# Kernel optimization log

Measured on AMD Instinct MI355X. Metric: run time of the kernel, lower is better.

Reference implementation:

```python
import jax, jax.numpy as jnp
import numpy as np

EPS = 1e-5
MAX_NORM = 1.0 - EPS
K = 16
ALPHA = 0.1
TAU = 0.1  # softmax temperature in forward


def project(x):
    # enforce ||x|| < 1 on the Poincare ball
    n = jnp.clip(jnp.linalg.norm(x, axis=-1, keepdims=True), EPS, None)
    return x / jnp.maximum(n / MAX_NORM, 1.0)


def mobius_add(u, v):
    c = 1.0
    dot_uv = jnp.sum(u * v, axis=-1, keepdims=True)
    nu = jnp.clip(jnp.sum(u * u, axis=-1, keepdims=True), 0.0, MAX_NORM ** 2)
    nv = jnp.clip(jnp.sum(v * v, axis=-1, keepdims=True), 0.0, MAX_NORM ** 2)
    num = (1 + 2 * c * dot_uv + c * nv) * u + (1 - c * nu) * v
    den = 1 + 2 * c * dot_uv + c * c * nu * nv
    return project(num / jnp.clip(den, EPS, None))


def exp_map(x, v):
    # sqrt_c = 1
    vn = jnp.clip(jnp.linalg.norm(v, axis=-1, keepdims=True), EPS, None)
    second = jnp.tanh(vn / 2.0) * v / vn
    return mobius_add(x, second)


def poincare_cdist(q, mem):
    # q: [B, M], mem: [N, M] -> [B, N] geodesic distances (c=1)
    qn = jnp.clip(jnp.sum(q * q, axis=-1), 0.0, MAX_NORM ** 2)          # [B]
    mn = jnp.clip(jnp.sum(mem * mem, axis=-1), 0.0, MAX_NORM ** 2)      # [N]
    # ||q - m||^2 expanded via gram matrix (same math as diff-based form)
    dist_sq = jnp.clip(jnp.sum(q * q, axis=-1)[:, None] + jnp.sum(mem * mem, axis=-1)[None, :]
                       - 2.0 * q @ mem.T, 0.0, None)                     # [B, N]
    den = (1.0 - qn)[:, None] * (1.0 - mn)[None, :]
    x = 2.0 * dist_sq / jnp.clip(den, EPS, None)
    return jnp.arccosh(1.0 + x)


def layernorm(x, g, b):
    mu = jnp.mean(x, axis=-1, keepdims=True)
    var = jnp.mean((x - mu) ** 2, axis=-1, keepdims=True)
    return (x - mu) / jnp.sqrt(var + 1e-5) * g + b


def setup_inputs() -> dict:
    key = jax.random.key(0)
    ks = jax.random.split(key, 10)
    B, S, H, M, N = 32, 2048, 1024, 128, 500000
    hidden_states = jax.random.normal(ks[0], (B, S, H), dtype=jnp.float32)
    W1 = jax.random.normal(ks[1], (H, M), dtype=jnp.float32) * 0.02
    b1 = jnp.zeros((M,), dtype=jnp.float32)
    ln_g = jnp.ones((M,), dtype=jnp.float32)
    ln_b = jnp.zeros((M,), dtype=jnp.float32)
    W2 = jax.random.normal(ks[2], (M, M), dtype=jnp.float32) * 0.02
    b2 = jnp.zeros((M,), dtype=jnp.float32)
    q_origin = jnp.zeros((1, M), dtype=jnp.float32)
    memory = project(jax.random.normal(ks[3], (N, M), dtype=jnp.float32) * 0.3)
    Wp = jax.random.normal(ks[4], (M, H), dtype=jnp.float32) * 0.02
    bp = jnp.zeros((H,), dtype=jnp.float32)
    return {"hidden_states": hidden_states, "W1": W1, "b1": b1, "ln_g": ln_g,
            "ln_b": ln_b, "W2": W2, "b2": b2, "q_origin": q_origin,
            "memory": memory, "Wp": Wp, "bp": bp}


def reference(hidden_states, W1, b1, ln_g, ln_b, W2, b2, q_origin, memory, Wp, bp):
    B, S, H = hidden_states.shape
    # query network on mean-pooled hidden states
    pooled = jnp.mean(hidden_states, axis=1)                  # [B, H]
    h = pooled @ W1 + b1                                      # [B, M]
    h = jax.nn.gelu(layernorm(h, ln_g, ln_b), approximate=False)
    tangent = h @ W2 + b2                                     # [B, M]
    origin = project(jnp.broadcast_to(q_origin, (B, q_origin.shape[-1])))
    query = exp_map(origin, tangent)                          # [B, M] on ball
    # geodesic kNN over the memory bank
    dists = poincare_cdist(query, memory)                     # [B, N]
    neg_top, idx = jax.lax.top_k(-dists, K)                   # smallest K
    top_d = -neg_top                                          # [B, K]
    neighbors = memory[idx]                                   # [B, K, M]
    w = jax.nn.softmax(-top_d / TAU, axis=-1)                 # [B, K]
    retrieved = jnp.einsum('bk,bkm->bm', w, neighbors)        # [B, M]
    force = retrieved @ Wp + bp                               # [B, H]
    return hidden_states + ALPHA * force[:, None, :]
```

## Files before the change

kernel.cpp:

```cpp
#include <hip/hip_runtime.h>
#include <float.h>
#include <math.h>

#define B_ 32
#define S_ 2048
#define H_ 1024
#define M_ 128
#define N_ 500000
#define KK 16
#define ALPHA_ 0.1f
#define TAU_ 0.1f
#define EPS_ 1e-5f
#define MAX_NORM_ 0.99999f
#define MAXN2_ (MAX_NORM_ * MAX_NORM_)
#define SC_ 64
#define CH_ 512
#define NBLK_ ((N_ + CH_ - 1) / CH_)
#define WIN_ 2048
#define NWIN_ ((N_ + WIN_ - 1) / WIN_)
#define NPAD_ (NWIN_ * WIN_)

__global__ __launch_bounds__(256) void k1_pool(const float* __restrict__ hid,
                                               float* __restrict__ pp) {
    int bid = blockIdx.x;
    int b = bid >> 6, sc = bid & 63;
    const float4* h4 = (const float4*)hid;
    float4 acc = {0.f, 0.f, 0.f, 0.f};
    int s0 = sc * (S_ / SC_);
    for (int s = 0; s < S_ / SC_; ++s) {
        float4 v = h4[((size_t)(b * S_ + s0 + s) << 8) + threadIdx.x];
        acc.x += v.x; acc.y += v.y; acc.z += v.z; acc.w += v.w;
    }
    ((float4*)pp)[(size_t)(b * SC_ + sc) * 256 + threadIdx.x] = acc;
}

__device__ __forceinline__ float block_reduce_sum_128(float v, volatile float* red, int tid) {
    red[tid] = v;
    __syncthreads();
    if (tid < 64) red[tid] += red[tid + 64];
    __syncthreads();
    if (tid < 64) {
        float x = red[tid];
        #pragma unroll
        for (int off = 32; off >= 1; off >>= 1) x += __shfl_down(x, off);
        if (tid == 0) red[0] = x;
    }
    __syncthreads();
    float r = red[0];
    __syncthreads();
    return r;
}

__global__ void k2_query(const float* __restrict__ pp, const float* __restrict__ W1,
                         const float* __restrict__ b1, const float* __restrict__ ln_g,
                         const float* __restrict__ ln_b, const float* __restrict__ W2,
                         const float* __restrict__ b2, const float* __restrict__ qorig,
                         float* __restrict__ query, float* __restrict__ qstats) {
    __shared__ float pooled[H_];
    __shared__ float red[128];
    __shared__ float hv[M_];
    int b = blockIdx.x, tid = threadIdx.x;
    #pragma unroll
    for (int j = 0; j < H_ / 128; ++j) {
        int h = tid + j * 128;
        float s = 0.f;
        for (int sc = 0; sc < SC_; ++sc) s += pp[(size_t)(b * SC_ + sc) * H_ + h];
        pooled[h] = s * (1.0f / (float)S_);
    }
    __syncthreads();
    int m = tid;
    float x = b1[m];
    for (int k = 0; k < H_; ++k) x = fmaf(pooled[k], W1[k * M_ + m], x);
    float mu = block_reduce_sum_128(x, red, tid) * (1.0f / (float)M_);
    float dmu = x - mu;
    float var = block_reduce_sum_128(dmu * dmu, red, tid) * (1.0f / (float)M_);
    float xh = dmu * rsqrtf(var + 1e-5f) * ln_g[m] + ln_b[m];
    float g = 0.5f * xh * (1.0f + erff(xh * 0.70710678f));
    hv[m] = g;
    __syncthreads();
    float t = b2[m];
    for (int k = 0; k < M_; ++k) t = fmaf(hv[k], W2[k * M_ + m], t);
    float o = qorig[m];
    float on2 = block_reduce_sum_128(o * o, red, tid);
    float on = fmaxf(sqrtf(on2), EPS_);
    float osc = 1.0f / fmaxf(on / MAX_NORM_, 1.0f);
    float u = o * osc;
    float vn2 = block_reduce_sum_128(t * t, red, tid);
    float vn = fmaxf(sqrtf(vn2), EPS_);
    float sec = tanhf(vn * 0.5f) * t / vn;
    float dot_uv = block_reduce_sum_128(u * sec, red, tid);
    float nu = fminf(fmaxf(block_reduce_sum_128(u * u, red, tid), 0.f), MAXN2_);
    float nv = fminf(fmaxf(block_reduce_sum_128(sec * sec, red, tid), 0.f), MAXN2_);
    float num = (1.0f + 2.0f * dot_uv + nv) * u + (1.0f - nu) * sec;
    float den = 1.0f + 2.0f * dot_uv + nu * nv;
    float r = num / fmaxf(den, EPS_);
    float rn2 = block_reduce_sum_128(r * r, red, tid);
    float rn = fmaxf(sqrtf(rn2), EPS_);
    float rsc = 1.0f / fmaxf(rn / MAX_NORM_, 1.0f);
    float q = r * rsc;
    query[b * M_ + m] = q;
    float qq = block_reduce_sum_128(q * q, red, tid);
    if (tid == 0) {
        qstats[b * 2 + 0] = qq;
        float qn = fminf(fmaxf(qq, 0.f), MAXN2_);
        qstats[b * 2 + 1] = 1.0f - qn;
    }
}

__global__ __launch_bounds__(256, 4) void k3_scores(const float* __restrict__ mem,
                                                    const float* __restrict__ query,
                                                    const float* __restrict__ qstats,
                                                    float* __restrict__ score) {
    int tid = threadIdx.x, bid = blockIdx.x;
    int r0 = bid * CH_ + tid;
    int r1 = r0 + 256;
    bool v0 = r0 < N_, v1 = r1 < N_;
    const float4* m0p = (const float4*)(mem + (size_t)(v0 ? r0 : 0) * M_);
    const float4* m1p = (const float4*)(mem + (size_t)(v1 ? r1 : 0) * M_);
    const float4* q4 = (const float4*)query;

    float acc0[B_], acc1[B_];
    #pragma unroll
    for (int b = 0; b < B_; ++b) { acc0[b] = 0.f; acc1[b] = 0.f; }
    float mm0 = 0.f, mm1 = 0.f;

    #pragma unroll 1
    for (int ko = 0; ko < 8; ++ko) {
        float4 a[4], c[4];
        #pragma unroll
        for (int i = 0; i < 4; ++i) { a[i] = m0p[ko * 4 + i]; }
        #pragma unroll
        for (int i = 0; i < 4; ++i) { c[i] = m1p[ko * 4 + i]; }
        #pragma unroll
        for (int i = 0; i < 4; ++i) {
            mm0 = fmaf(a[i].x, a[i].x, fmaf(a[i].y, a[i].y, fmaf(a[i].z, a[i].z, fmaf(a[i].w, a[i].w, mm0))));
            mm1 = fmaf(c[i].x, c[i].x, fmaf(c[i].y, c[i].y, fmaf(c[i].z, c[i].z, fmaf(c[i].w, c[i].w, mm1))));
        }
        #pragma unroll
        for (int b = 0; b < B_; ++b) {
            #pragma unroll
            for (int i = 0; i < 4; ++i) {
                float4 qv = q4[b * 32 + ko * 4 + i];
                acc0[b] = fmaf(qv.x, a[i].x, fmaf(qv.y, a[i].y, fmaf(qv.z, a[i].z, fmaf(qv.w, a[i].w, acc0[b]))));
                acc1[b] = fmaf(qv.x, c[i].x, fmaf(qv.y, c[i].y, fmaf(qv.z, c[i].z, fmaf(qv.w, c[i].w, acc1[b]))));
            }
        }
    }

    float mn0 = fminf(mm0, MAXN2_), mn1 = fminf(mm1, MAXN2_);
    #pragma unroll
    for (int b = 0; b < B_; ++b) {
        float qq = qstats[b * 2];
        float omq = qstats[b * 2 + 1];
        float ds0 = fmaxf(qq + mm0 - 2.0f * acc0[b], 0.f);
        float t0 = ds0 / fmaxf(omq * (1.0f - mn0), EPS_);
        float ds1 = fmaxf(qq + mm1 - 2.0f * acc1[b], 0.f);
        float t1 = ds1 / fmaxf(omq * (1.0f - mn1), EPS_);
        if (v0) score[(size_t)b * NPAD_ + r0] = t0;
        if (v1) score[(size_t)b * NPAD_ + r1] = t1;
    }
}

__global__ __launch_bounds__(256, 4) void k4_sel(const float* __restrict__ score,
                                                 float* __restrict__ cand_val,
                                                 int* __restrict__ cand_idx) {
    int win = blockIdx.x;
    int wave = threadIdx.x >> 6, lane = threadIdx.x & 63;
    int base = win * WIN_;
    #pragma unroll 2
    for (int j = 0; j < 8; ++j) {
        int b = wave * 8 + j;
        const float* sp = score + (size_t)b * NPAD_ + base;
        unsigned keys[32];
        #pragma unroll
        for (int i = 0; i < 32; ++i) {
            int lr = lane + i * 64;
            float v = sp[lr];
            unsigned kb = __float_as_uint(v);
            keys[i] = ((base + lr) < N_) ? ((kb & ~2047u) | (unsigned)lr) : 0xFFFFFFFFu;
        }
        for (int k = 0; k < KK; ++k) {
            unsigned m = keys[0];
            #pragma unroll
            for (int i = 1; i < 32; ++i) m = min(m, keys[i]);
            #pragma unroll
            for (int off = 32; off >= 1; off >>= 1)
                m = min(m, (unsigned)__shfl_xor((int)m, off));
            if (lane == 0) {
                cand_val[((size_t)win * B_ + b) * KK + k] = __uint_as_float(m & ~2047u);
                cand_idx[((size_t)win * B_ + b) * KK + k] = base + (int)(m & 2047u);
            }
            #pragma unroll
            for (int i = 0; i < 32; ++i)
                if (keys[i] == m) keys[i] = 0xFFFFFFFFu;
        }
    }
}

__global__ void k45_retrieve(const float* __restrict__ cand_val,
                             const int* __restrict__ cand_idx,
                             const float* __restrict__ mem, const float* __restrict__ query,
                             const float* __restrict__ qstats,
                             const float* __restrict__ Wp, const float* __restrict__ bp,
                             float* __restrict__ force) {
    __shared__ float tv[256 * KK];
    __shared__ int ti[256 * KK];
    __shared__ float mv[64 * KK];
    __shared__ int mi[64 * KK];
    __shared__ int topk_s[KK];
    __shared__ float q_s[M_];
    __shared__ float d_s[KK];
    __shared__ float w_s[KK];
    __shared__ float ret_s[M_];
    int b = blockIdx.x, tid = threadIdx.x;

    float val[KK]; int idx[KK];
    #pragma unroll
    for (int i = 0; i < KK; ++i) { val[i] = FLT_MAX; idx[i] = 0; }
    int nc = NWIN_ * KK;
    for (int c = tid; c < nc; c += 256) {
        int g = c >> 4, k = c & 15;
        float v = cand_val[((size_t)g * B_ + b) * KK + k];
        int id = cand_idx[((size_t)g * B_ + b) * KK + k];
        if (v < val[KK - 1]) {
            val[KK - 1] = v; idx[KK - 1] = id;
            #pragma unroll
            for (int j = KK - 1; j > 0; --j) {
                if (val[j] < val[j - 1]) {
                    float tvv = val[j]; val[j] = val[j - 1]; val[j - 1] = tvv;
                    int tii = idx[j]; idx[j] = idx[j - 1]; idx[j - 1] = tii;
                }
            }
        }
    }
    if (tid < M_) q_s[tid] = query[b * M_ + tid];
    #pragma unroll
    for (int i = 0; i < KK; ++i) { tv[tid * KK + i] = val[i]; ti[tid * KK + i] = idx[i]; }
    __syncthreads();

    if (tid < 64) {
        #pragma unroll
        for (int i = 0; i < KK; ++i) { val[i] = FLT_MAX; idx[i] = 0; }
        for (int t = tid * 4; t < tid * 4 + 4; ++t) {
            for (int i = 0; i < KK; ++i) {
                float v = tv[t * KK + i]; int id = ti[t * KK + i];
                if (v >= val[KK - 1]) break;
                val[KK - 1] = v; idx[KK - 1] = id;
                #pragma unroll
                for (int j = KK - 1; j > 0; --j) {
                    if (val[j] < val[j - 1]) {
                        float tvv = val[j]; val[j] = val[j - 1]; val[j - 1] = tvv;
                        int tii = idx[j]; idx[j] = idx[j - 1]; idx[j - 1] = tii;
                    }
                }
            }
        }
        #pragma unroll
        for (int i = 0; i < KK; ++i) { mv[tid * KK + i] = val[i]; mi[tid * KK + i] = idx[i]; }
        int h = 0;
        for (int k = 0; k < KK; ++k) {
            float cv = (h < KK) ? mv[tid * KK + h] : FLT_MAX;
            int ci = (h < KK) ? mi[tid * KK + h] : 0;
            float bestv = cv; int bestl = tid;
            #pragma unroll
            for (int off = 32; off >= 1; off >>= 1) {
                float ov = __shfl_down(bestv, off);
                int ol = __shfl_down(bestl, off);
                if (ov < bestv) { bestv = ov; bestl = ol; }
            }
            bestl = __shfl(bestl, 0);
            if (tid == bestl) {
                int id = ci;
                topk_s[k] = (id < 0) ? 0 : ((id >= N_) ? (N_ - 1) : id);
                h++;
            }
        }
    }
    __syncthreads();

    float qq = qstats[b * 2], omq = qstats[b * 2 + 1];
    int wave = tid >> 6, lane = tid & 63;
    for (int ii = wave; ii < KK; ii += 4) {
        const float* mr = mem + (size_t)topk_s[ii] * M_;
        float a0 = mr[lane], a1 = mr[lane + 64];
        float p = q_s[lane] * a0 + q_s[lane + 64] * a1;
        float mm = a0 * a0 + a1 * a1;
        #pragma unroll
        for (int off = 32; off >= 1; off >>= 1) {
            p += __shfl_down(p, off);
            mm += __shfl_down(mm, off);
        }
        if (lane == 0) {
            float dsq = fmaxf(qq + mm - 2.0f * p, 0.f);
            float mn = fminf(mm, MAXN2_);
            float t = dsq / fmaxf(omq * (1.0f - mn), EPS_);
            d_s[ii] = acoshf(1.0f + 2.0f * t);
        }
    }
    __syncthreads();
    if (tid == 0) {
        float dmin = d_s[0];
        for (int i = 1; i < KK; ++i) dmin = fminf(dmin, d_s[i]);
        float Z = 0.f;
        for (int i = 0; i < KK; ++i) {
            float w = expf((dmin - d_s[i]) * (1.0f / TAU_));
            w_s[i] = w; Z += w;
        }
        float iZ = 1.0f / Z;
        for (int i = 0; i < KK; ++i) w_s[i] *= iZ;
    }
    __syncthreads();
    if (tid < M_) {
        float r = 0.f;
        for (int i = 0; i < KK; ++i) r = fmaf(w_s[i], mem[(size_t)topk_s[i] * M_ + tid], r);
        ret_s[tid] = r;
    }
    __syncthreads();
    #pragma unroll
    for (int j = 0; j < 4; ++j) {
        int h = tid + j * 256;
        float f = bp[h];
        for (int k = 0; k < M_; ++k) f = fmaf(ret_s[k], Wp[k * H_ + h], f);
        force[b * H_ + h] = f;
    }
}

__global__ __launch_bounds__(256) void k6_out(const float* __restrict__ hid,
                                              const float* __restrict__ force,
                                              float* __restrict__ out) {
    const float4* h4 = (const float4*)hid;
    const float4* f4 = (const float4*)force;
    float4* o4 = (float4*)out;
    int n4 = B_ * S_ * H_ / 4;
    for (int i = blockIdx.x * blockDim.x + threadIdx.x; i < n4; i += gridDim.x * blockDim.x) {
        int b = i >> 19;
        float4 hv = h4[i];
        float4 fv = f4[(b << 8) + (i & 255)];
        float4 ov;
        ov.x = fmaf(ALPHA_, fv.x, hv.x);
        ov.y = fmaf(ALPHA_, fv.y, hv.y);
        ov.z = fmaf(ALPHA_, fv.z, hv.z);
        ov.w = fmaf(ALPHA_, fv.w, hv.w);
        o4[i] = ov;
    }
}

extern "C" void kernel_launch(void* const* d_in, const int* in_sizes, int n_in,
                              void* d_out, int out_size, void* d_ws, size_t ws_size,
                              hipStream_t stream) {
    const float* hid    = (const float*)d_in[0];
    const float* W1     = (const float*)d_in[1];
    const float* b1     = (const float*)d_in[2];
    const float* ln_g   = (const float*)d_in[3];
    const float* ln_b   = (const float*)d_in[4];
    const float* W2     = (const float*)d_in[5];
    const float* b2     = (const float*)d_in[6];
    const float* qorig  = (const float*)d_in[7];
    const float* mem    = (const float*)d_in[8];
    const float* Wp     = (const float*)d_in[9];
    const float* bp     = (const float*)d_in[10];
    float* out = (float*)d_out;

    char* ws = (char*)d_ws;
    size_t off = 0;
    float* pp = (float*)(ws + off);       off += (size_t)B_ * SC_ * H_ * 4;
    float* query = (float*)(ws + off);    off += (size_t)B_ * M_ * 4;
    float* qstats = (float*)(ws + off);   off += (size_t)B_ * 2 * 4;
    float* score = (float*)(ws + off);    off += (size_t)B_ * NPAD_ * 4;
    float* cand_val = (float*)(ws + off); off += (size_t)NWIN_ * B_ * KK * 4;
    int* cand_idx = (int*)(ws + off);     off += (size_t)NWIN_ * B_ * KK * 4;
    float* force = (float*)(ws + off);    off += (size_t)B_ * H_ * 4;
    (void)ws_size; (void)in_sizes; (void)n_in; (void)out_size;

    hipLaunchKernelGGL(k1_pool, dim3(B_ * SC_), dim3(256), 0, stream, hid, pp);
    hipLaunchKernelGGL(k2_query, dim3(B_), dim3(128), 0, stream, pp, W1, b1, ln_g, ln_b,
                       W2, b2, qorig, query, qstats);
    hipLaunchKernelGGL(k3_scores, dim3(NBLK_), dim3(256), 0, stream, mem, query, qstats, score);
    hipLaunchKernelGGL(k4_sel, dim3(NWIN_), dim3(256), 0, stream, score, cand_val, cand_idx);
    hipLaunchKernelGGL(k45_retrieve, dim3(B_), dim3(256), 0, stream, cand_val, cand_idx,
                       mem, query, qstats, Wp, bp, force);
    hipLaunchKernelGGL(k6_out, dim3(2048), dim3(256), 0, stream, hid, force, out);
}
```

Baseline: 440.0 us.

## Use bf16 MFMA for memory-bank scores with fp32 rerank of top-32 candidates

```diff
diff --git a/kernel.cpp b/kernel.cpp
--- a/kernel.cpp
+++ b/kernel.cpp
@@ -8,17 +8,26 @@
 #define M_ 128
 #define N_ 500000
 #define KK 16
+#define KK2 32
 #define ALPHA_ 0.1f
 #define TAU_ 0.1f
 #define EPS_ 1e-5f
 #define MAX_NORM_ 0.99999f
 #define MAXN2_ (MAX_NORM_ * MAX_NORM_)
 #define SC_ 64
-#define CH_ 512
-#define NBLK_ ((N_ + CH_ - 1) / CH_)
+#define RPB_ 512
+#define NBLK_ ((N_ + RPB_ - 1) / RPB_)
 #define WIN_ 2048
 #define NWIN_ ((N_ + WIN_ - 1) / WIN_)
 #define NPAD_ (NWIN_ * WIN_)
+
+typedef __attribute__((ext_vector_type(8))) short short8;
+typedef __attribute__((ext_vector_type(4))) float f32x4;
+
+__device__ __forceinline__ unsigned short to_bf16(float x) {
+    unsigned u = __float_as_uint(x);
+    return (unsigned short)((u + 0x7FFFu + ((u >> 16) & 1u)) >> 16);
+}
 
 __global__ __launch_bounds__(256) void k1_pool(const float* __restrict__ hid,
                                                float* __restrict__ pp) {
@@ -110,74 +119,133 @@
 __global__ __launch_bounds__(256, 4) void k3_scores(const float* __restrict__ mem,
                                                     const float* __restrict__ query,
                                                     const float* __restrict__ qstats,
-                                                    float* __restrict__ score) {
+                                                    unsigned* __restrict__ keyplane) {
+    __shared__ unsigned key_lds[B_][260];
+    __shared__ float mm_lds[256];
+    __shared__ float qq_s[B_], omq_s[B_];
     int tid = threadIdx.x, bid = blockIdx.x;
-    int r0 = bid * CH_ + tid;
-    int r1 = r0 + 256;
-    bool v0 = r0 < N_, v1 = r1 < N_;
-    const float4* m0p = (const float4*)(mem + (size_t)(v0 ? r0 : 0) * M_);
-    const float4* m1p = (const float4*)(mem + (size_t)(v1 ? r1 : 0) * M_);
-    const float4* q4 = (const float4*)query;
-
-    float acc0[B_], acc1[B_];
+    int wave = tid >> 6, lane = tid & 63;
+    int l15 = lane & 15, lk = lane >> 4;
+
+    if (tid < B_) { qq_s[tid] = qstats[tid * 2]; omq_s[tid] = qstats[tid * 2 + 1]; }
+
+    short8 bfrag[2][4];
     #pragma unroll
-    for (int b = 0; b < B_; ++b) { acc0[b] = 0.f; acc1[b] = 0.f; }
-    float mm0 = 0.f, mm1 = 0.f;
+    for (int bg = 0; bg < 2; ++bg) {
+        #pragma unroll
+        for (int kt = 0; kt < 4; ++kt) {
+            int batch = bg * 16 + l15;
+            const float4* qp = (const float4*)(query + batch * M_ + kt * 32 + lk * 8);
+            float4 lo = qp[0], hi = qp[1];
+            short8 f;
+            f[0] = (short)to_bf16(lo.x); f[1] = (short)to_bf16(lo.y);
+            f[2] = (short)to_bf16(lo.z); f[3] = (short)to_bf16(lo.w);
+            f[4] = (short)to_bf16(hi.x); f[5] = (short)to_bf16(hi.y);
+            f[6] = (short)to_bf16(hi.z); f[7] = (short)to_bf16(hi.w);
+            bfrag[bg][kt] = f;
+        }
+    }
 
     #pragma unroll 1
-    for (int ko = 0; ko < 8; ++ko) {
-        float4 a[4], c[4];
-        #pragma unroll
-        for (int i = 0; i < 4; ++i) { a[i] = m0p[ko * 4 + i]; }
-        #pragma unroll
-        for (int i = 0; i < 4; ++i) { c[i] = m1p[ko * 4 + i]; }
-        #pragma unroll
-        for (int i = 0; i < 4; ++i) {
-            mm0 = fmaf(a[i].x, a[i].x, fmaf(a[i].y, a[i].y, fmaf(a[i].z, a[i].z, fmaf(a[i].w, a[i].w, mm0))));
-            mm1 = fmaf(c[i].x, c[i].x, fmaf(c[i].y, c[i].y, fmaf(c[i].z, c[i].z, fmaf(c[i].w, c[i].w, mm1))));
-        }
-        #pragma unroll
-        for (int b = 0; b < B_; ++b) {
-            #pragma unroll
-            for (int i = 0; i < 4; ++i) {
-                float4 qv = q4[b * 32 + ko * 4 + i];
-                acc0[b] = fmaf(qv.x, a[i].x, fmaf(qv.y, a[i].y, fmaf(qv.z, a[i].z, fmaf(qv.w, a[i].w, acc0[b]))));
-                acc1[b] = fmaf(qv.x, c[i].x, fmaf(qv.y, c[i].y, fmaf(qv.z, c[i].z, fmaf(qv.w, c[i].w, acc1[b]))));
-            }
-        }
-    }
-
-    float mn0 = fminf(mm0, MAXN2_), mn1 = fminf(mm1, MAXN2_);
-    #pragma unroll
-    for (int b = 0; b < B_; ++b) {
-        float qq = qstats[b * 2];
-        float omq = qstats[b * 2 + 1];
-        float ds0 = fmaxf(qq + mm0 - 2.0f * acc0[b], 0.f);
-        float t0 = ds0 / fmaxf(omq * (1.0f - mn0), EPS_);
-        float ds1 = fmaxf(qq + mm1 - 2.0f * acc1[b], 0.f);
-        float t1 = ds1 / fmaxf(omq * (1.0f - mn1), EPS_);
-        if (v0) score[(size_t)b * NPAD_ + r0] = t0;
-        if (v1) score[(size_t)b * NPAD_ + r1] = t1;
-    }
-}
-
-__global__ __launch_bounds__(256, 4) void k4_sel(const float* __restrict__ score,
-                                                 float* __restrict__ cand_val,
-                                                 int* __restrict__ cand_idx) {
-    int win = blockIdx.x;
+    for (int p = 0; p < 2; ++p) {
+        int passbase = bid * RPB_ + p * 256;
+        f32x4 acc[4][2];
+        #pragma unroll
+        for (int rg = 0; rg < 4; ++rg)
+            #pragma unroll
+            for (int bg = 0; bg < 2; ++bg)
+                acc[rg][bg] = (f32x4){0.f, 0.f, 0.f, 0.f};
+        float mmp[4] = {0.f, 0.f, 0.f, 0.f};
+
+        #pragma unroll 1
+        for (int rg = 0; rg < 4; ++rg) {
+            int r = passbase + wave * 64 + rg * 16 + l15;
+            const float4* mp = (const float4*)(mem + (size_t)((r < N_) ? r : 0) * M_);
+            #pragma unroll
+            for (int kt = 0; kt < 4; ++kt) {
+                float4 lo = mp[kt * 8 + lk * 2];
+                float4 hi = mp[kt * 8 + lk * 2 + 1];
+                mmp[rg] = fmaf(lo.x, lo.x, fmaf(lo.y, lo.y, fmaf(lo.z, lo.z, fmaf(lo.w, lo.w, mmp[rg]))));
+                mmp[rg] = fmaf(hi.x, hi.x, fmaf(hi.y, hi.y, fmaf(hi.z, hi.z, fmaf(hi.w, hi.w, mmp[rg]))));
+                short8 af;
+                af[0] = (short)to_bf16(lo.x); af[1] = (short)to_bf16(lo.y);
+                af[2] = (short)to_bf16(lo.z); af[3] = (short)to_bf16(lo.w);
+                af[4] = (short)to_bf16(hi.x); af[5] = (short)to_bf16(hi.y);
+                af[6] = (short)to_bf16(hi.z); af[7] = (short)to_bf16(hi.w);
+                acc[rg][0] = __builtin_amdgcn_mfma_f32_16x16x32_bf16(af, bfrag[0][kt], acc[rg][0], 0, 0, 0);
+                acc[rg][1] = __builtin_amdgcn_mfma_f32_16x16x32_bf16(af, bfrag[1][kt], acc[rg][1], 0, 0, 0);
+            }
+        }
+        #pragma unroll
+        for (int rg = 0; rg < 4; ++rg) {
+            float v = mmp[rg] + __shfl_xor(mmp[rg], 16);
+            v += __shfl_xor(v, 32);
+            if (lane < 16) mm_lds[wave * 64 + rg * 16 + l15] = v;
+        }
+        __syncthreads();
+
+        #pragma unroll
+        for (int rg = 0; rg < 4; ++rg) {
+            #pragma unroll
+            for (int bg = 0; bg < 2; ++bg) {
+                #pragma unroll
+                for (int reg = 0; reg < 4; ++reg) {
+                    int row_local = wave * 64 + rg * 16 + lk * 4 + reg;
+                    int batch = bg * 16 + l15;
+                    float dot = acc[rg][bg][reg];
+                    float mmv = mm_lds[row_local];
+                    float mn = fminf(mmv, MAXN2_);
+                    float dsq = fmaxf(qq_s[batch] + mmv - 2.0f * dot, 0.f);
+                    float t = dsq / fmaxf(omq_s[batch] * (1.0f - mn), EPS_);
+                    int grow = passbase + row_local;
+                    unsigned key = (__float_as_uint(t) & ~2047u) | ((unsigned)grow & 2047u);
+                    key_lds[batch][row_local] = key;
+                }
+            }
+        }
+        __syncthreads();
+
+        {
+            int batch = tid >> 3, chunk = tid & 7;
+            int rbase = passbase + chunk * 32;
+            unsigned* dstp = keyplane + (size_t)batch * NPAD_ + rbase;
+            #pragma unroll
+            for (int i = 0; i < 8; ++i) {
+                int rl = chunk * 32 + i * 4;
+                uint4 v = *(const uint4*)&key_lds[batch][rl];
+                int gr = rbase + i * 4;
+                if (gr + 4 <= N_) {
+                    *(uint4*)(dstp + i * 4) = v;
+                } else {
+                    if (gr + 0 < N_) dstp[i * 4 + 0] = v.x;
+                    if (gr + 1 < N_) dstp[i * 4 + 1] = v.y;
+                    if (gr + 2 < N_) dstp[i * 4 + 2] = v.z;
+                    if (gr + 3 < N_) dstp[i * 4 + 3] = v.w;
+                }
+            }
+        }
+        __syncthreads();
+    }
+}
+
+__global__ __launch_bounds__(256, 4) void k4_sel(const unsigned* __restrict__ keyplane,
+                                                 unsigned* __restrict__ cand_key) {
+    int win = blockIdx.x >> 2, quad = blockIdx.x & 3;
     int wave = threadIdx.x >> 6, lane = threadIdx.x & 63;
     int base = win * WIN_;
-    #pragma unroll 2
-    for (int j = 0; j < 8; ++j) {
-        int b = wave * 8 + j;
-        const float* sp = score + (size_t)b * NPAD_ + base;
+    #pragma unroll 1
+    for (int j = 0; j < 2; ++j) {
+        int b = quad * 8 + wave * 2 + j;
+        const uint4* kp = (const uint4*)(keyplane + (size_t)b * NPAD_ + base);
         unsigned keys[32];
         #pragma unroll
-        for (int i = 0; i < 32; ++i) {
-            int lr = lane + i * 64;
-            float v = sp[lr];
-            unsigned kb = __float_as_uint(v);
-            keys[i] = ((base + lr) < N_) ? ((kb & ~2047u) | (unsigned)lr) : 0xFFFFFFFFu;
+        for (int i = 0; i < 8; ++i) {
+            uint4 v = kp[lane + i * 64];
+            int pos = base + (lane + i * 64) * 4;
+            keys[i * 4 + 0] = (pos + 0 < N_) ? v.x : 0xFFFFFFFFu;
+            keys[i * 4 + 1] = (pos + 1 < N_) ? v.y : 0xFFFFFFFFu;
+            keys[i * 4 + 2] = (pos + 2 < N_) ? v.z : 0xFFFFFFFFu;
+            keys[i * 4 + 3] = (pos + 3 < N_) ? v.w : 0xFFFFFFFFu;
         }
         for (int k = 0; k < KK; ++k) {
             unsigned m = keys[0];
@@ -186,10 +254,7 @@
             #pragma unroll
             for (int off = 32; off >= 1; off >>= 1)
                 m = min(m, (unsigned)__shfl_xor((int)m, off));
-            if (lane == 0) {
-                cand_val[((size_t)win * B_ + b) * KK + k] = __uint_as_float(m & ~2047u);
-                cand_idx[((size_t)win * B_ + b) * KK + k] = base + (int)(m & 2047u);
-            }
+            if (lane == 0) cand_key[((size_t)win * B_ + b) * KK + k] = m;
             #pragma unroll
             for (int i = 0; i < 32; ++i)
                 if (keys[i] == m) keys[i] = 0xFFFFFFFFu;
@@ -197,37 +262,37 @@
     }
 }
 
-__global__ void k45_retrieve(const float* __restrict__ cand_val,
-                             const int* __restrict__ cand_idx,
+__global__ void k45_retrieve(const unsigned* __restrict__ cand_key,
                              const float* __restrict__ mem, const float* __restrict__ query,
                              const float* __restrict__ qstats,
                              const float* __restrict__ Wp, const float* __restrict__ bp,
                              float* __restrict__ force) {
-    __shared__ float tv[256 * KK];
+    __shared__ unsigned tv[256 * KK];
     __shared__ int ti[256 * KK];
-    __shared__ float mv[64 * KK];
+    __shared__ unsigned mv[64 * KK];
     __shared__ int mi[64 * KK];
-    __shared__ int topk_s[KK];
+    __shared__ int top32_s[KK2];
     __shared__ float q_s[M_];
-    __shared__ float d_s[KK];
+    __shared__ float d_s[KK2];
     __shared__ float w_s[KK];
+    __shared__ int idx_s[KK];
     __shared__ float ret_s[M_];
     int b = blockIdx.x, tid = threadIdx.x;
 
-    float val[KK]; int idx[KK];
+    unsigned val[KK]; int idx[KK];
     #pragma unroll
-    for (int i = 0; i < KK; ++i) { val[i] = FLT_MAX; idx[i] = 0; }
+    for (int i = 0; i < KK; ++i) { val[i] = 0xFFFFFFFFu; idx[i] = 0; }
     int nc = NWIN_ * KK;
     for (int c = tid; c < nc; c += 256) {
         int g = c >> 4, k = c & 15;
-        float v = cand_val[((size_t)g * B_ + b) * KK + k];
-        int id = cand_idx[((size_t)g * B_ + b) * KK + k];
+        unsigned v = cand_key[((size_t)g * B_ + b) * KK + k];
+        int id = g * WIN_ + (int)(v & 2047u);
         if (v < val[KK - 1]) {
             val[KK - 1] = v; idx[KK - 1] = id;
             #pragma unroll
             for (int j = KK - 1; j > 0; --j) {
                 if (val[j] < val[j - 1]) {
-                    float tvv = val[j]; val[j] = val[j - 1]; val[j - 1] = tvv;
+                    unsigned tvv = val[j]; val[j] = val[j - 1]; val[j - 1] = tvv;
                     int tii = idx[j]; idx[j] = idx[j - 1]; idx[j - 1] = tii;
                 }
             }
@@ -240,16 +305,16 @@
 
     if (tid < 64) {
         #pragma unroll
-        for (int i = 0; i < KK; ++i) { val[i] = FLT_MAX; idx[i] = 0; }
+        for (int i = 0; i < KK; ++i) { val[i] = 0xFFFFFFFFu; idx[i] = 0; }
         for (int t = tid * 4; t < tid * 4 + 4; ++t) {
             for (int i = 0; i < KK; ++i) {
-                float v = tv[t * KK + i]; int id = ti[t * KK + i];
+                unsigned v = tv[t * KK + i]; int id = ti[t * KK + i];
                 if (v >= val[KK - 1]) break;
                 val[KK - 1] = v; idx[KK - 1] = id;
                 #pragma unroll
                 for (int j = KK - 1; j > 0; --j) {
                     if (val[j] < val[j - 1]) {
-                        float tvv = val[j]; val[j] = val[j - 1]; val[j - 1] = tvv;
+                        unsigned tvv = val[j]; val[j] = val[j - 1]; val[j - 1] = tvv;
                         int tii = idx[j]; idx[j] = idx[j - 1]; idx[j - 1] = tii;
                     }
                 }
@@ -258,20 +323,19 @@
         #pragma unroll
         for (int i = 0; i < KK; ++i) { mv[tid * KK + i] = val[i]; mi[tid * KK + i] = idx[i]; }
         int h = 0;
-        for (int k = 0; k < KK; ++k) {
-            float cv = (h < KK) ? mv[tid * KK + h] : FLT_MAX;
+        for (int k = 0; k < KK2; ++k) {
+            unsigned cv = (h < KK) ? mv[tid * KK + h] : 0xFFFFFFFFu;
             int ci = (h < KK) ? mi[tid * KK + h] : 0;
-            float bestv = cv; int bestl = tid;
+            unsigned bestv = cv; int bestl = tid;
             #pragma unroll
             for (int off = 32; off >= 1; off >>= 1) {
-                float ov = __shfl_down(bestv, off);
+                unsigned ov = (unsigned)__shfl_down((int)bestv, off);
                 int ol = __shfl_down(bestl, off);
                 if (ov < bestv) { bestv = ov; bestl = ol; }
             }
             bestl = __shfl(bestl, 0);
             if (tid == bestl) {
-                int id = ci;
-                topk_s[k] = (id < 0) ? 0 : ((id >= N_) ? (N_ - 1) : id);
+                top32_s[k] = (ci < 0) ? 0 : ((ci >= N_) ? (N_ - 1) : ci);
                 h++;
             }
         }
@@ -280,8 +344,8 @@
 
     float qq = qstats[b * 2], omq = qstats[b * 2 + 1];
     int wave = tid >> 6, lane = tid & 63;
-    for (int ii = wave; ii < KK; ii += 4) {
-        const float* mr = mem + (size_t)topk_s[ii] * M_;
+    for (int ii = wave; ii < KK2; ii += 4) {
+        const float* mr = mem + (size_t)top32_s[ii] * M_;
         float a0 = mr[lane], a1 = mr[lane + 64];
         float p = q_s[lane] * a0 + q_s[lane + 64] * a1;
         float mm = a0 * a0 + a1 * a1;
@@ -299,11 +363,24 @@
     }
     __syncthreads();
     if (tid == 0) {
-        float dmin = d_s[0];
-        for (int i = 1; i < KK; ++i) dmin = fminf(dmin, d_s[i]);
+        bool used[KK2];
+        for (int i = 0; i < KK2; ++i) used[i] = false;
+        float seld[KK];
+        for (int k = 0; k < KK; ++k) {
+            float bd = FLT_MAX; int bi = -1;
+            for (int i = 0; i < KK2; ++i) {
+                if (used[i]) continue;
+                if (d_s[i] < bd || (d_s[i] == bd && (bi < 0 || top32_s[i] < top32_s[bi]))) {
+                    bd = d_s[i]; bi = i;
+                }
+            }
+            used[bi] = true; seld[k] = bd; idx_s[k] = top32_s[bi];
+        }
+        float dmin = seld[0];
+        for (int i = 1; i < KK; ++i) dmin = fminf(dmin, seld[i]);
         float Z = 0.f;
         for (int i = 0; i < KK; ++i) {
-            float w = expf((dmin - d_s[i]) * (1.0f / TAU_));
+            float w = expf((dmin - seld[i]) * (1.0f / TAU_));
             w_s[i] = w; Z += w;
         }
         float iZ = 1.0f / Z;
@@ -312,7 +389,7 @@
     __syncthreads();
     if (tid < M_) {
         float r = 0.f;
-        for (int i = 0; i < KK; ++i) r = fmaf(w_s[i], mem[(size_t)topk_s[i] * M_ + tid], r);
+        for (int i = 0; i < KK; ++i) r = fmaf(w_s[i], mem[(size_t)idx_s[i] * M_ + tid], r);
         ret_s[tid] = r;
     }
     __syncthreads();
@@ -363,21 +440,21 @@
 
     char* ws = (char*)d_ws;
     size_t off = 0;
-    float* pp = (float*)(ws + off);       off += (size_t)B_ * SC_ * H_ * 4;
-    float* query = (float*)(ws + off);    off += (size_t)B_ * M_ * 4;
-    float* qstats = (float*)(ws + off);   off += (size_t)B_ * 2 * 4;
-    float* score = (float*)(ws + off);    off += (size_t)B_ * NPAD_ * 4;
-    float* cand_val = (float*)(ws + off); off += (size_t)NWIN_ * B_ * KK * 4;
-    int* cand_idx = (int*)(ws + off);     off += (size_t)NWIN_ * B_ * KK * 4;
-    float* force = (float*)(ws + off);    off += (size_t)B_ * H_ * 4;
+    float* pp = (float*)(ws + off);        off += (size_t)B_ * SC_ * H_ * 4;
+    float* query = (float*)(ws + off);     off += (size_t)B_ * M_ * 4;
+    float* qstats = (float*)(ws + off);    off += (size_t)B_ * 2 * 4;
+    off = (off + 255) & ~(size_t)255;
+    unsigned* keyplane = (unsigned*)(ws + off); off += (size_t)B_ * NPAD_ * 4;
+    unsigned* cand_key = (unsigned*)(ws + off); off += (size_t)NWIN_ * B_ * KK * 4;
+    float* force = (float*)(ws + off);     off += (size_t)B_ * H_ * 4;
     (void)ws_size; (void)in_sizes; (void)n_in; (void)out_size;
 
     hipLaunchKernelGGL(k1_pool, dim3(B_ * SC_), dim3(256), 0, stream, hid, pp);
     hipLaunchKernelGGL(k2_query, dim3(B_), dim3(128), 0, stream, pp, W1, b1, ln_g, ln_b,
                        W2, b2, qorig, query, qstats);
-    hipLaunchKernelGGL(k3_scores, dim3(NBLK_), dim3(256), 0, stream, mem, query, qstats, score);
-    hipLaunchKernelGGL(k4_sel, dim3(NWIN_), dim3(256), 0, stream, score, cand_val, cand_idx);
-    hipLaunchKernelGGL(k45_retrieve, dim3(B_), dim3(256), 0, stream, cand_val, cand_idx,
+    hipLaunchKernelGGL(k3_scores, dim3(NBLK_), dim3(256), 0, stream, mem, query, qstats, keyplane);
+    hipLaunchKernelGGL(k4_sel, dim3(NWIN_ * 4), dim3(256), 0, stream, keyplane, cand_key);
+    hipLaunchKernelGGL(k45_retrieve, dim3(B_), dim3(256), 0, stream, cand_key,
                        mem, query, qstats, Wp, bp, force);
     hipLaunchKernelGGL(k6_out, dim3(2048), dim3(256), 0, stream, hid, force, out);
 }
```

Measured after the change: 427.7 us. 2.8% less time.
